# Performance work log

Measured on AMD Instinct MI355X. Metric: run time of the kernel, lower is better.

## Reference

```python
import jax, jax.numpy as jnp
import numpy as np

IN_CH, OUT_CH, K = 4096, 4096, 64
C, F = IN_CH // K, OUT_CH // K  # 64, 64
BS = 256


def setup_inputs() -> dict:
    key = jax.random.key(0)
    k1, k2 = jax.random.split(key)
    x = jax.random.normal(k1, (BS, IN_CH), dtype=jnp.float32)
    stdv = 1.0 / float(np.sqrt(C))  # matches torch init: uniform(-1/sqrt(in_channels), ...)
    weights = jax.random.uniform(k2, (F, C, K), dtype=jnp.float32, minval=-stdv, maxval=stdv)
    return {"x": x, "weights": weights}


def reference(x, weights):
    # Faithful, batched version of Linear_BC_func.forward:
    #   per sample: ifft(fft(w, 'ortho') * fft(x, 'backward'), 'ortho').real, summed over C.
    # The per-sample Python loop and the C-sum are fused: sum over C is done in the
    # frequency domain (linearity of ifft), and the batch is handled by one einsum.
    bs = x.shape[0]
    f, c, k = weights.shape
    xk = x.reshape(bs, c, k)
    Wf = jnp.fft.fft(weights, norm="ortho")      # (F, C, K) complex64
    Xf = jnp.fft.fft(xk, norm="backward")        # (BS, C, K) complex64
    Sf = jnp.einsum("fck,bck->bfk", Wf, Xf)      # sum over C in frequency domain
    out = jnp.fft.ifft(Sf, norm="ortho").real.astype(jnp.float32)  # torch .float() keeps real part
    return out.reshape(bs, f * k)
```

## Files before the change

### kernel.cpp

```cpp
#include <hip/hip_runtime.h>


#define KDIM 4096

typedef __attribute__((ext_vector_type(8)))  short s16x8;
typedef __attribute__((ext_vector_type(4)))  float f32x4;
typedef __attribute__((ext_vector_type(16))) float f32x16;
typedef unsigned short u16;

__device__ __forceinline__ u16 f2bf(float f) {
  unsigned int u = __float_as_uint(f);
  u += 0x7FFF + ((u >> 16) & 1);
  return (u16)(u >> 16);
}

__global__ __launch_bounds__(256) void pack_kernel(const float* __restrict__ x,
                                                   u16* __restrict__ Xp) {
  int g   = blockIdx.x * 256 + threadIdx.x;
  int row = g >> 9;
  int k8  = g & 511;
  const float4* src = (const float4*)(x + ((size_t)row << 12) + (k8 << 3));
  float4 v0 = src[0], v1 = src[1];
  union { u16 u[8]; uint4 v; } o;
  o.u[0] = f2bf(v0.x); o.u[1] = f2bf(v0.y); o.u[2] = f2bf(v0.z); o.u[3] = f2bf(v0.w);
  o.u[4] = f2bf(v1.x); o.u[5] = f2bf(v1.y); o.u[6] = f2bf(v1.z); o.u[7] = f2bf(v1.w);
  int c  = k8 >> 3;
  int r3 = k8 & 7;
  int kk = r3 >> 1;
  int lh = r3 & 1;
  int lane = (lh << 5) | (row & 31);
  int rg = row >> 5;
  size_t u = ((size_t)((c * 8 + rg) * 4 + kk) << 6) + lane;
  *(uint4*)(Xp + (u << 3)) = o.v;
}

__global__ __launch_bounds__(1024) void gemm_direct(const u16* __restrict__ Xp,
                                                    const float* __restrict__ w,
                                                    float* __restrict__ out) {
  extern __shared__ __align__(16) char pool[];
  __shared__ __align__(16) u16 Cs[2][8][576];

  const int tid   = threadIdx.x;
  const int lane  = tid & 63;
  const int wid   = tid >> 6;
  const int cslot = wid & 7;
  const int half  = wid >> 3;
  const int l31   = lane & 31;
  const int lh    = lane >> 5;
  const int f     = blockIdx.x >> 2;
  const int q     = blockIdx.x & 3;
  const int rg    = q * 2 + half;

  int bofs[4];
  #pragma unroll
  for (int s = 0; s < 4; ++s) {
    int i0 = (lh * 8 - l31 - 16 * s) & 63;
    bofs[s] = (i0 & 7) * 72 + (i0 & ~7);
  }

  const u16* abase = Xp + ((size_t)(cslot * 8 + rg) * 4 * 512 + lane * 8);

  const float* wrow = w + ((size_t)f << 12) + (cslot << 6) + lane;

  if (half == 0) {
    u16 bv = f2bf(wrow[0]);
    #pragma unroll
    for (int m = 0; m < 8; ++m) {
      int i = (-(lane + m)) & 63;
      Cs[0][cslot][m * 72 + i] = bv;
    }
  }

  f32x16 acc0 = {}, acc1 = {};
  s16x8 a[4], an[4];
  #pragma unroll
  for (int kk = 0; kk < 4; ++kk)
    a[kk] = *(const s16x8*)(abase + kk * 512);

  __syncthreads();

  for (int t = 0; t < 8; ++t) {
    const u16* T = &Cs[t & 1][cslot][0];
    float vw;
    if (t < 7) {
      if (half == 0) vw = wrow[(t + 1) * 512];
      #pragma unroll
      for (int kk = 0; kk < 4; ++kk)
        an[kk] = *(const s16x8*)(abase + (size_t)(t + 1) * 131072 + kk * 512);
    }
    s16x8 b[4];
    #pragma unroll
    for (int s = 0; s < 4; ++s)
      b[s] = *(const s16x8*)(T + bofs[s]);
    #pragma unroll
    for (int kk = 0; kk < 4; ++kk) {
      acc0 = __builtin_amdgcn_mfma_f32_32x32x16_bf16(a[kk], b[(0 - kk) & 3], acc0, 0, 0, 0);
      acc1 = __builtin_amdgcn_mfma_f32_32x32x16_bf16(a[kk], b[(2 - kk) & 3], acc1, 0, 0, 0);
    }
    if (t < 7) {
      if (half == 0) {
        u16 nb = f2bf(vw);
        #pragma unroll
        for (int m = 0; m < 8; ++m) {
          int i = (-(lane + m)) & 63;
          Cs[(t + 1) & 1][cslot][m * 72 + i] = nb;
        }
      }
      #pragma unroll
      for (int kk = 0; kk < 4; ++kk) a[kk] = an[kk];
    }
    __syncthreads();
  }

  float* red = (float*)pool;
  {
    float* r0 = red + ((size_t)(wid * 2 + 0) * 64 + lane) * 16;
    float* r1 = red + ((size_t)(wid * 2 + 1) * 64 + lane) * 16;
    #pragma unroll
    for (int i = 0; i < 4; ++i) {
      f32x4 v0 = {acc0[4 * i], acc0[4 * i + 1], acc0[4 * i + 2], acc0[4 * i + 3]};
      f32x4 v1 = {acc1[4 * i], acc1[4 * i + 1], acc1[4 * i + 2], acc1[4 * i + 3]};
      *(f32x4*)(r0 + 4 * i) = v0;
      *(f32x4*)(r1 + 4 * i) = v1;
    }
  }
  __syncthreads();
  {
    int rq  = tid & 3;
    int ln  = (tid >> 2) & 63;
    int nn2 = (tid >> 8) & 1;
    int hf  = tid >> 9;
    f32x4 s = {};
    #pragma unroll
    for (int cs = 0; cs < 8; ++cs)
      s += *(const f32x4*)(red + ((size_t)(((hf * 8 + cs) * 2) + nn2) * 64 + ln) * 16 + rq * 4);
    int colg = f * 64 + nn2 * 32 + (ln & 31);
    int rowb = q * 64 + hf * 32 + 8 * rq + 4 * (ln >> 5);
    #pragma unroll
    for (int e = 0; e < 4; ++e)
      out[(size_t)(rowb + e) * 4096 + colg] = s[e];
  }
}

extern "C" void kernel_launch(void* const* d_in, const int* in_sizes, int n_in,
                              void* d_out, int out_size, void* d_ws, size_t ws_size,
                              hipStream_t stream) {
  const float* x = (const float*)d_in[0];
  const float* w = (const float*)d_in[1];
  float* out = (float*)d_out;

  u16* Xp = (u16*)d_ws;

  pack_kernel<<<512, 256, 0, stream>>>(x, Xp);
  gemm_direct<<<256, 1024, 131072, stream>>>(Xp, w, out);
}
```

Baseline: 21.25 us.

## Preload full circulant weight table to LDS and remove per-step barriers

All 64 weight circulant tables for the output block are built in shared memory up front by all 16 waves, so the k-loop needs no per-iteration __syncthreads or double-buffered weight staging. The loop is fully unrolled with explicit register prefetch of the A fragments. The cross-wave reduction becomes a tree reduction through a smaller LDS buffer, and the final store is done directly from wave 0's registers. Dynamic LDS drops from 128KB to 72KB. In exchange, the tree reduction adds several barriers and leaves most waves idle at the end, and the final global stores are less coalesced.

```diff
diff --git a/kernel.cpp b/kernel.cpp
--- a/kernel.cpp
+++ b/kernel.cpp
@@ -34,11 +34,11 @@
   *(uint4*)(Xp + (u << 3)) = o.v;
 }
 
-__global__ __launch_bounds__(1024) void gemm_direct(const u16* __restrict__ Xp,
-                                                    const float* __restrict__ w,
-                                                    float* __restrict__ out) {
+__global__ __launch_bounds__(1024, 4) void gemm_free(const u16* __restrict__ Xp,
+                                                     const float* __restrict__ w,
+                                                     float* __restrict__ out) {
   extern __shared__ __align__(16) char pool[];
-  __shared__ __align__(16) u16 Cs[2][8][576];
+  u16* tab = (u16*)pool;
 
   const int tid   = threadIdx.x;
   const int lane  = tid & 63;
@@ -51,94 +51,107 @@
   const int q     = blockIdx.x & 3;
   const int rg    = q * 2 + half;
 
+  const float* wf = w + ((size_t)f << 12);
+  #pragma unroll
+  for (int j = 0; j < 4; ++j) {
+    int c = wid * 4 + j;
+    u16 bv = f2bf(wf[(c << 6) + lane]);
+    u16* T = tab + c * 576;
+    #pragma unroll
+    for (int m = 0; m < 8; ++m) {
+      int i = (-(lane + m)) & 63;
+      T[m * 72 + i] = bv;
+    }
+  }
+
   int bofs[4];
   #pragma unroll
   for (int s = 0; s < 4; ++s) {
     int i0 = (lh * 8 - l31 - 16 * s) & 63;
-    bofs[s] = (i0 & 7) * 72 + (i0 & ~7);
+    bofs[s] = (i0 & 7) * 71 + i0;
   }
 
-  const u16* abase = Xp + ((size_t)(cslot * 8 + rg) * 4 * 512 + lane * 8);
-
-  const float* wrow = w + ((size_t)f << 12) + (cslot << 6) + lane;
-
-  if (half == 0) {
-    u16 bv = f2bf(wrow[0]);
-    #pragma unroll
-    for (int m = 0; m < 8; ++m) {
-      int i = (-(lane + m)) & 63;
-      Cs[0][cslot][m * 72 + i] = bv;
-    }
-  }
+  const u16* abase = Xp + ((size_t)(cslot * 8 + rg) * 2048 + lane * 8);
 
   f32x16 acc0 = {}, acc1 = {};
-  s16x8 a[4], an[4];
-  #pragma unroll
-  for (int kk = 0; kk < 4; ++kk)
-    a[kk] = *(const s16x8*)(abase + kk * 512);
+  s16x8 a0, a1, a2, a3, n0, n1, n2, n3;
+  a0 = *(const s16x8*)(abase);
+  a1 = *(const s16x8*)(abase + 512);
+  a2 = *(const s16x8*)(abase + 1024);
+  a3 = *(const s16x8*)(abase + 1536);
 
   __syncthreads();
 
+  #pragma unroll
   for (int t = 0; t < 8; ++t) {
-    const u16* T = &Cs[t & 1][cslot][0];
-    float vw;
     if (t < 7) {
-      if (half == 0) vw = wrow[(t + 1) * 512];
-      #pragma unroll
-      for (int kk = 0; kk < 4; ++kk)
-        an[kk] = *(const s16x8*)(abase + (size_t)(t + 1) * 131072 + kk * 512);
+      const u16* nb = abase + (size_t)(t + 1) * 131072;
+      n0 = *(const s16x8*)(nb);
+      n1 = *(const s16x8*)(nb + 512);
+      n2 = *(const s16x8*)(nb + 1024);
+      n3 = *(const s16x8*)(nb + 1536);
     }
-    s16x8 b[4];
-    #pragma unroll
-    for (int s = 0; s < 4; ++s)
-      b[s] = *(const s16x8*)(T + bofs[s]);
-    #pragma unroll
-    for (int kk = 0; kk < 4; ++kk) {
-      acc0 = __builtin_amdgcn_mfma_f32_32x32x16_bf16(a[kk], b[(0 - kk) & 3], acc0, 0, 0, 0);
-      acc1 = __builtin_amdgcn_mfma_f32_32x32x16_bf16(a[kk], b[(2 - kk) & 3], acc1, 0, 0, 0);
-    }
-    if (t < 7) {
-      if (half == 0) {
-        u16 nb = f2bf(vw);
-        #pragma unroll
-        for (int m = 0; m < 8; ++m) {
-          int i = (-(lane + m)) & 63;
-          Cs[(t + 1) & 1][cslot][m * 72 + i] = nb;
-        }
-      }
-      #pragma unroll
-      for (int kk = 0; kk < 4; ++kk) a[kk] = an[kk];
-    }
-    __syncthreads();
+    const u16* T = tab + (8 * t + cslot) * 576;
+    s16x8 b0 = *(const s16x8*)(T + bofs[0]);
+    s16x8 b1 = *(const s16x8*)(T + bofs[1]);
+    s16x8 b2 = *(const s16x8*)(T + bofs[2]);
+    s16x8 b3 = *(const s16x8*)(T + bofs[3]);
+    acc0 = __builtin_amdgcn_mfma_f32_32x32x16_bf16(a0, b0, acc0, 0, 0, 0);
+    acc1 = __builtin_amdgcn_mfma_f32_32x32x16_bf16(a0, b2, acc1, 0, 0, 0);
+    acc0 = __builtin_amdgcn_mfma_f32_32x32x16_bf16(a1, b3, acc0, 0, 0, 0);
+    acc1 = __builtin_amdgcn_mfma_f32_32x32x16_bf16(a1, b1, acc1, 0, 0, 0);
+    acc0 = __builtin_amdgcn_mfma_f32_32x32x16_bf16(a2, b2, acc0, 0, 0, 0);
+    acc1 = __builtin_amdgcn_mfma_f32_32x32x16_bf16(a2, b0, acc1, 0, 0, 0);
+    acc0 = __builtin_amdgcn_mfma_f32_32x32x16_bf16(a3, b1, acc0, 0, 0, 0);
+    acc1 = __builtin_amdgcn_mfma_f32_32x32x16_bf16(a3, b3, acc1, 0, 0, 0);
+    if (t < 7) { a0 = n0; a1 = n1; a2 = n2; a3 = n3; }
   }
 
+  __syncthreads();
   float* red = (float*)pool;
-  {
-    float* r0 = red + ((size_t)(wid * 2 + 0) * 64 + lane) * 16;
-    float* r1 = red + ((size_t)(wid * 2 + 1) * 64 + lane) * 16;
+
+  #define WRITE_ACC(k)                                                        \
+    { float* Bf = red + (size_t)(half * 4 + (k)) * 2048;                      \
+      _Pragma("unroll")                                                       \
+      for (int i = 0; i < 4; ++i) {                                           \
+        f32x4 v0 = {acc0[4*i], acc0[4*i+1], acc0[4*i+2], acc0[4*i+3]};        \
+        f32x4 v1 = {acc1[4*i], acc1[4*i+1], acc1[4*i+2], acc1[4*i+3]};        \
+        *(f32x4*)(Bf + (size_t)i * 256 + lane * 4) = v0;                      \
+        *(f32x4*)(Bf + (size_t)(i + 4) * 256 + lane * 4) = v1;                \
+      } }
+  #define ADD_ACC(k)                                                          \
+    { const float* Bf = red + (size_t)(half * 4 + (k)) * 2048;                \
+      _Pragma("unroll")                                                       \
+      for (int i = 0; i < 4; ++i) {                                           \
+        f32x4 v0 = *(const f32x4*)(Bf + (size_t)i * 256 + lane * 4);          \
+        f32x4 v1 = *(const f32x4*)(Bf + (size_t)(i + 4) * 256 + lane * 4);    \
+        _Pragma("unroll")                                                     \
+        for (int e = 0; e < 4; ++e) {                                         \
+          acc0[4*i+e] += v0[e];                                               \
+          acc1[4*i+e] += v1[e];                                               \
+        }                                                                     \
+      } }
+
+  if (cslot >= 4) WRITE_ACC(cslot - 4);
+  __syncthreads();
+  if (cslot < 4) ADD_ACC(cslot);
+  __syncthreads();
+  if (cslot == 2 || cslot == 3) WRITE_ACC(cslot - 2);
+  __syncthreads();
+  if (cslot < 2) ADD_ACC(cslot);
+  __syncthreads();
+  if (cslot == 1) WRITE_ACC(0);
+  __syncthreads();
+  if (cslot == 0) {
+    ADD_ACC(0);
+    const int colg = (f << 6) + l31;
+    const int rowb = q * 64 + half * 32 + 4 * lh;
     #pragma unroll
-    for (int i = 0; i < 4; ++i) {
-      f32x4 v0 = {acc0[4 * i], acc0[4 * i + 1], acc0[4 * i + 2], acc0[4 * i + 3]};
-      f32x4 v1 = {acc1[4 * i], acc1[4 * i + 1], acc1[4 * i + 2], acc1[4 * i + 3]};
-      *(f32x4*)(r0 + 4 * i) = v0;
-      *(f32x4*)(r1 + 4 * i) = v1;
+    for (int r = 0; r < 16; ++r) {
+      int row = rowb + (r & 3) + 8 * (r >> 2);
+      out[(size_t)row * 4096 + colg]      = acc0[r];
+      out[(size_t)row * 4096 + colg + 32] = acc1[r];
     }
-  }
-  __syncthreads();
-  {
-    int rq  = tid & 3;
-    int ln  = (tid >> 2) & 63;
-    int nn2 = (tid >> 8) & 1;
-    int hf  = tid >> 9;
-    f32x4 s = {};
-    #pragma unroll
-    for (int cs = 0; cs < 8; ++cs)
-      s += *(const f32x4*)(red + ((size_t)(((hf * 8 + cs) * 2) + nn2) * 64 + ln) * 16 + rq * 4);
-    int colg = f * 64 + nn2 * 32 + (ln & 31);
-    int rowb = q * 64 + hf * 32 + 8 * rq + 4 * (ln >> 5);
-    #pragma unroll
-    for (int e = 0; e < 4; ++e)
-      out[(size_t)(rowb + e) * 4096 + colg] = s[e];
   }
 }
 
@@ -152,5 +165,5 @@
   u16* Xp = (u16*)d_ws;
 
   pack_kernel<<<512, 256, 0, stream>>>(x, Xp);
-  gemm_direct<<<256, 1024, 131072, stream>>>(Xp, w, out);
+  gemm_free<<<256, 1024, 73728, stream>>>(Xp, w, out);
 }
```

Result: no change. 21.22 us (-0.1%).
